# Kernel optimization log

Measured on AMD Instinct MI355X. Metric: run time of the kernel, lower is better.

Reference implementation:

```python
import jax, jax.numpy as jnp
import numpy as np

B, N, DIM = 4, 4096, 1024
HEADS, DIM_HEAD, BSZ, EPS = 8, 64, 16, 1e-8
INNER = HEADS * DIM_HEAD


def setup_inputs() -> dict:
    key = jax.random.key(0)
    k1, k2, k3 = jax.random.split(key, 3)
    x = jax.random.normal(k1, (B, N, DIM), dtype=jnp.float32)
    # torch nn.Linear weights are [out, in]; scale ~ fan_in^-0.5 for stable exp()
    w_qkv = jax.random.normal(k2, (3 * INNER, DIM), dtype=jnp.float32) * (DIM ** -0.5)
    w_out = jax.random.normal(k3, (DIM, INNER), dtype=jnp.float32) * (INNER ** -0.5)
    b_out = jnp.zeros((DIM,), dtype=jnp.float32)
    return {"x": x, "w_qkv": w_qkv, "w_out": w_out, "b_out": b_out}


def _to_bh(t, b, n):
    # 'b n (h d) -> (b h) n d'
    return t.reshape(b, n, HEADS, DIM_HEAD).transpose(0, 2, 1, 3).reshape(b * HEADS, n, DIM_HEAD)


def _to_blocks(t):
    # 'b (n z) d -> b n z d'
    return t.reshape(t.shape[0], -1, BSZ, DIM_HEAD)


def _calc_Y_and_A(qb, kb, vb):
    S = jnp.einsum('bnid,bnjd->bnij', qb, kb)   # block-local scores
    A = jnp.exp(S)
    y = jnp.einsum('bnij,bnjd->bnid', A, vb)
    return y.reshape(y.shape[0], -1, DIM_HEAD), A.sum(-1).reshape(A.shape[0], -1)


def _hattention(x, w_qkv, w_out, b_out):
    b, n, _ = x.shape
    qkv = x @ w_qkv.T
    q, k, v = jnp.split(qkv, 3, axis=-1)
    q, k, v = (_to_bh(t, b, n) for t in (q, k, v))
    q = q * (DIM_HEAD ** -0.5)

    num_levels = int(np.log2(n // BSZ)) - 1
    qkvs = [(q, k, v)]
    for _ in range(num_levels):
        q = q.reshape(q.shape[0], -1, 2, DIM_HEAD).mean(axis=2)
        k = k.reshape(k.shape[0], -1, 2, DIM_HEAD).mean(axis=2)
        v = v.reshape(v.shape[0], -1, 2, DIM_HEAD).sum(axis=2)
        qkvs.append((q, k, v))
    top_level = qkvs[0]
    coarse_levels = qkvs[1:][::-1]  # coarsest first

    Ys = []
    for (ql, kl, vl) in coarse_levels:
        qb, kb, vb = map(_to_blocks, (ql, kl, vl))
        bh, nb = kb.shape[0], kb.shape[1]
        # flip sibling key blocks: 'b (n r) z d' with r=2 reversed
        kb = kb.reshape(bh, nb // 2, 2, BSZ, DIM_HEAD)[:, :, ::-1].reshape(bh, nb, BSZ, DIM_HEAD)
        Ys.append(_calc_Y_and_A(qb, kb, vb))
    Ys.append(_calc_Y_and_A(*map(_to_blocks, top_level)))

    Y, A = Ys[0]
    for y_l, a_l in Ys[1:]:
        Y = jnp.repeat(Y, 2, axis=1) + y_l
        A = jnp.repeat(A, 2, axis=1) + a_l

    out = Y / (A + EPS)[..., None]
    # '(b h) n d -> b n (h d)'
    out = out.reshape(b, HEADS, n, DIM_HEAD).transpose(0, 2, 1, 3).reshape(b, n, INNER)
    return out @ w_out.T + b_out


def reference(x, w_qkv, w_out, b_out):
    return _hattention(x, w_qkv, w_out, b_out)
```

## Files before the change

kernel.cpp:

```cpp
#include <hip/hip_runtime.h>
#include <hip/hip_bf16.h>


typedef __bf16 bf16x8 __attribute__((ext_vector_type(8)));
typedef float floatx4 __attribute__((ext_vector_type(4)));
typedef unsigned short ushortx8 __attribute__((ext_vector_type(8)));
typedef unsigned int uintx4 __attribute__((ext_vector_type(4)));

#define ROWS_PER_BH 8160

__device__ __forceinline__ void g2lds16(const void* g, void* l) {
  __builtin_amdgcn_global_load_lds(
      (const __attribute__((address_space(1))) void*)g,
      (__attribute__((address_space(3))) void*)l, 16, 0, 0);
}

__device__ __forceinline__ unsigned short f2bu(float x) {
  __hip_bfloat16 h = __float2bfloat16(x);
  return *(unsigned short*)&h;
}
__device__ __forceinline__ float bu2f(unsigned short u) {
  __hip_bfloat16 h = *(__hip_bfloat16*)&u;
  return __bfloat162float(h);
}

__global__ __launch_bounds__(256) void f2b_kernel(const float* __restrict__ s,
                                                  __hip_bfloat16* __restrict__ d,
                                                  int n) {
  int i0 = (blockIdx.x * 256 + threadIdx.x) * 4;
  if (i0 + 3 < n) {
    float4 v = *(const float4*)(s + i0);
    d[i0 + 0] = __float2bfloat16(v.x);
    d[i0 + 1] = __float2bfloat16(v.y);
    d[i0 + 2] = __float2bfloat16(v.z);
    d[i0 + 3] = __float2bfloat16(v.w);
  }
}

template <int K>
__device__ __forceinline__ void gemm_core(const unsigned short* __restrict__ A,
                                          const unsigned short* __restrict__ B,
                                          unsigned short* ldsA, unsigned short* ldsB,
                                          int tM, int tN, floatx4 acc[4][4]) {
  const int tid = threadIdx.x;
  const int lane = tid & 63, w = tid >> 6;
  const int wm = w >> 1, wn = w & 1;
  const int lr = lane >> 3;
  const int gch = (lane & 7) ^ lr;
  const unsigned short* Ag = A + (size_t)(tM + w * 32 + lr) * K + gch * 8;
  const unsigned short* Bg = B + (size_t)(tN + w * 32 + lr) * K + gch * 8;
  unsigned short* lA = &ldsA[w * 2048 + lane * 8];
  unsigned short* lB = &ldsB[w * 2048 + lane * 8];

  const int rA = wm * 64 + (lane & 15);
  const int rB = wn * 64 + (lane & 15);
  const int quad = lane >> 4;
  const int sw = lane & 7;

  for (int kt = 0; kt < K; kt += 64) {
    __syncthreads();
#pragma unroll
    for (int c = 0; c < 4; c++) {
      g2lds16(Ag + (size_t)(c * 8) * K + kt, lA + c * 512);
      g2lds16(Bg + (size_t)(c * 8) * K + kt, lB + c * 512);
    }
    __syncthreads();
#pragma unroll
    for (int kk = 0; kk < 2; kk++) {
      bf16x8 af[4], bv[4];
#pragma unroll
      for (int i = 0; i < 4; i++)
        af[i] = *(const bf16x8*)&ldsA[(rA + i * 16) * 64 + (((kk * 4 + quad) ^ sw) * 8)];
#pragma unroll
      for (int j = 0; j < 4; j++)
        bv[j] = *(const bf16x8*)&ldsB[(rB + j * 16) * 64 + (((kk * 4 + quad) ^ sw) * 8)];
#pragma unroll
      for (int i = 0; i < 4; i++)
#pragma unroll
        for (int j = 0; j < 4; j++)
          acc[i][j] = __builtin_amdgcn_mfma_f32_16x16x32_bf16(af[i], bv[j], acc[i][j], 0, 0, 0);
    }
  }
}

__global__ __launch_bounds__(256) void gemm_qkv_kernel(
    const unsigned short* __restrict__ A,
    const unsigned short* __restrict__ B,
    __hip_bfloat16* __restrict__ qp, __hip_bfloat16* __restrict__ kp,
    __hip_bfloat16* __restrict__ vp) {
  __shared__ unsigned short ldsA[128 * 64];
  __shared__ unsigned short ldsB[128 * 64];
  const int lane = threadIdx.x & 63, w = threadIdx.x >> 6;
  const int wm = w >> 1, wn = w & 1;
  const int tM = blockIdx.x * 128, tN = blockIdx.y * 128;

  floatx4 acc[4][4];
#pragma unroll
  for (int i = 0; i < 4; i++)
#pragma unroll
    for (int j = 0; j < 4; j++) acc[i][j] = (floatx4){0.f, 0.f, 0.f, 0.f};

  gemm_core<1024>(A, B, ldsA, ldsB, tM, tN, acc);

  const int quad = lane >> 4;
#pragma unroll
  for (int i = 0; i < 4; i++) {
#pragma unroll
    for (int j = 0; j < 4; j++) {
      const int c = tN + wn * 64 + j * 16 + (lane & 15);
      const int tensor = c >> 9;
      const int rem = c & 511;
      const int h = rem >> 6, d = rem & 63;
      __hip_bfloat16* dstbuf = (tensor == 0) ? qp : ((tensor == 1) ? kp : vp);
      const float scale = (tensor == 0) ? 0.125f : 1.0f;
#pragma unroll
      for (int r = 0; r < 4; r++) {
        const int m = tM + wm * 64 + i * 16 + quad * 4 + r;
        const int b = m >> 12, n = m & 4095;
        size_t dst = ((size_t)(b * 8 + h) * ROWS_PER_BH + n) * 64 + d;
        dstbuf[dst] = __float2bfloat16(acc[i][j][r] * scale);
      }
    }
  }
}

__global__ __launch_bounds__(256) void gemm_out_kernel(
    const unsigned short* __restrict__ A,
    const unsigned short* __restrict__ B,
    const float* __restrict__ bias, float* __restrict__ out) {
  __shared__ unsigned short ldsA[128 * 64];
  __shared__ unsigned short ldsB[128 * 64];
  const int lane = threadIdx.x & 63, w = threadIdx.x >> 6;
  const int wm = w >> 1, wn = w & 1;
  const int tM = blockIdx.x * 128, tN = blockIdx.y * 128;

  floatx4 acc[4][4];
#pragma unroll
  for (int i = 0; i < 4; i++)
#pragma unroll
    for (int j = 0; j < 4; j++) acc[i][j] = (floatx4){0.f, 0.f, 0.f, 0.f};

  gemm_core<512>(A, B, ldsA, ldsB, tM, tN, acc);

  const int quad = lane >> 4;
#pragma unroll
  for (int i = 0; i < 4; i++) {
#pragma unroll
    for (int j = 0; j < 4; j++) {
      const int c = tN + wn * 64 + j * 16 + (lane & 15);
      const float bb = bias[c];
#pragma unroll
      for (int r = 0; r < 4; r++) {
        const int m = tM + wm * 64 + i * 16 + quad * 4 + r;
        out[(size_t)m * 1024 + c] = acc[i][j][r] + bb;
      }
    }
  }
}

__global__ __launch_bounds__(256) void pyramid_all_kernel(
    __hip_bfloat16* __restrict__ qp, __hip_bfloat16* __restrict__ kp,
    __hip_bfloat16* __restrict__ vp) {
  __shared__ unsigned short qs[128 * 64], ks[128 * 64], vs[128 * 64];
  const int bh = blockIdx.x >> 5;
  const int chunk = blockIdx.x & 31;
  const int tid = threadIdx.x;
  const size_t base = (size_t)bh * ROWS_PER_BH;
  const size_t g0 = (base + chunk * 128) * 64;
  const unsigned short* qg = (const unsigned short*)qp;
  const unsigned short* kg = (const unsigned short*)kp;
  const unsigned short* vg = (const unsigned short*)vp;
#pragma unroll
  for (int c = 0; c < 4; c++) {
    int off = c * 2048 + tid * 8;
    *(ushortx8*)&qs[off] = *(const ushortx8*)(qg + g0 + off);
    *(ushortx8*)&ks[off] = *(const ushortx8*)(kg + g0 + off);
    *(ushortx8*)&vs[off] = *(const ushortx8*)(vg + g0 + off);
  }
  const int offs[8] = {0, 4096, 6144, 7168, 7680, 7936, 8064, 8128};
#pragma unroll
  for (int l = 1; l <= 7; l++) {
    __syncthreads();
    const int nOut = 128 >> l;
    for (int e = tid; e < nOut * 32; e += 256) {
      const int i = e >> 5, dp = (e & 31) * 2;
      const int a = (i << l) * 64 + dp;
      const int b = a + (1 << (l - 1)) * 64;
      unsigned short q0 = f2bu(0.5f * (bu2f(qs[a]) + bu2f(qs[b])));
      unsigned short q1 = f2bu(0.5f * (bu2f(qs[a + 1]) + bu2f(qs[b + 1])));
      unsigned short k0 = f2bu(0.5f * (bu2f(ks[a]) + bu2f(ks[b])));
      unsigned short k1 = f2bu(0.5f * (bu2f(ks[a + 1]) + bu2f(ks[b + 1])));
      unsigned short v0 = f2bu(bu2f(vs[a]) + bu2f(vs[b]));
      unsigned short v1 = f2bu(bu2f(vs[a + 1]) + bu2f(vs[b + 1]));
      qs[a] = q0; qs[a + 1] = q1;
      ks[a] = k0; ks[a + 1] = k1;
      vs[a] = v0; vs[a + 1] = v1;
      const size_t grow = (base + offs[l] + (size_t)chunk * nOut + i) * 64 + dp;
      *(unsigned int*)((unsigned short*)qp + grow) = (unsigned int)q0 | ((unsigned int)q1 << 16);
      *(unsigned int*)((unsigned short*)kp + grow) = (unsigned int)k0 | ((unsigned int)k1 << 16);
      *(unsigned int*)((unsigned short*)vp + grow) = (unsigned int)v0 | ((unsigned int)v1 << 16);
    }
  }
}

__global__ __launch_bounds__(256) void attn_kernel(
    const unsigned short* __restrict__ qp, const unsigned short* __restrict__ kp,
    const unsigned short* __restrict__ vp, __hip_bfloat16* __restrict__ yall,
    float* __restrict__ aall) {
  __shared__ __align__(16) unsigned short vT[4][64 * 24];
  const int w = threadIdx.x >> 6, lane = threadIdx.x & 63;
  const int g = blockIdx.x * 4 + w;
  if (g >= 510) return;
  const int bh = blockIdx.y;
  int level, blk;
  if (g < 256)      { level = 0; blk = g; }
  else if (g < 384) { level = 1; blk = g - 256; }
  else if (g < 448) { level = 2; blk = g - 384; }
  else if (g < 480) { level = 3; blk = g - 448; }
  else if (g < 496) { level = 4; blk = g - 480; }
  else if (g < 504) { level = 5; blk = g - 496; }
  else if (g < 508) { level = 6; blk = g - 504; }
  else              { level = 7; blk = g - 508; }
  const int ro = 8192 - (8192 >> level);
  const int kblk = (level == 0) ? blk : (blk ^ 1);
  const int m = lane & 15, q = lane >> 4;
  const size_t qbase = ((size_t)bh * ROWS_PER_BH + ro + blk * 16) * 64;
  const size_t kbase = ((size_t)bh * ROWS_PER_BH + ro + kblk * 16) * 64;

  const bf16x8 ka0 = *(const bf16x8*)(kp + kbase + m * 64 + q * 8);
  const bf16x8 ka1 = *(const bf16x8*)(kp + kbase + m * 64 + 32 + q * 8);
  const bf16x8 qb0 = *(const bf16x8*)(qp + qbase + m * 64 + q * 8);
  const bf16x8 qb1 = *(const bf16x8*)(qp + qbase + m * 64 + 32 + q * 8);

  const ushortx8 v0 = *(const ushortx8*)(vp + qbase + m * 64 + q * 16);
  const ushortx8 v1 = *(const ushortx8*)(vp + qbase + m * 64 + q * 16 + 8);
  unsigned short* vtw = vT[w];
#pragma unroll
  for (int j = 0; j < 8; j++) vtw[(q * 16 + j) * 24 + m] = v0[j];
#pragma unroll
  for (int j = 0; j < 8; j++) vtw[(q * 16 + 8 + j) * 24 + m] = v1[j];

  floatx4 s = (floatx4){0.f, 0.f, 0.f, 0.f};
  s = __builtin_amdgcn_mfma_f32_16x16x32_bf16(ka0, qb0, s, 0, 0, 0);
  s = __builtin_amdgcn_mfma_f32_16x16x32_bf16(ka1, qb1, s, 0, 0, 0);

  unsigned short pb0 = f2bu(__expf(s[0])), pb1 = f2bu(__expf(s[1]));
  unsigned short pb2 = f2bu(__expf(s[2])), pb3 = f2bu(__expf(s[3]));
  float asum = bu2f(pb0) + bu2f(pb1) + bu2f(pb2) + bu2f(pb3);
  asum += __shfl_xor(asum, 16, 64);
  asum += __shfl_xor(asum, 32, 64);
  const size_t arow = (size_t)bh * ROWS_PER_BH + ro + blk * 16;
  if (q == 0) aall[arow + m] = asum;

  unsigned int d0 = (unsigned int)pb0 | ((unsigned int)pb1 << 16);
  unsigned int d1 = (unsigned int)pb2 | ((unsigned int)pb3 << 16);
  const int s0l = m + 32 * (q & 1);
  unsigned int u0 = __shfl(d0, s0l, 64);
  unsigned int u1 = __shfl(d1, s0l, 64);
  unsigned int u2 = __shfl(d0, s0l + 16, 64);
  unsigned int u3 = __shfl(d1, s0l + 16, 64);
  union { uintx4 i; bf16x8 b; } pau;
  pau.i = (q < 2) ? (uintx4){u0, u1, u2, u3} : (uintx4){0u, 0u, 0u, 0u};
  const bf16x8 pa = pau.b;

#pragma unroll
  for (int c = 0; c < 4; c++) {
    union { uintx4 i; bf16x8 b; } bvu;
    bvu.i = (uintx4){0u, 0u, 0u, 0u};
    if (q < 2) bvu.b = *(const bf16x8*)&vtw[(c * 16 + m) * 24 + q * 8];
    floatx4 y = (floatx4){0.f, 0.f, 0.f, 0.f};
    y = __builtin_amdgcn_mfma_f32_16x16x32_bf16(pa, bvu.b, y, 0, 0, 0);
#pragma unroll
    for (int r = 0; r < 4; r++)
      yall[(arow + q * 4 + r) * 64 + c * 16 + m] = __float2bfloat16(y[r]);
  }
}

__global__ __launch_bounds__(256) void combine_kernel(
    const unsigned short* __restrict__ yall, const float* __restrict__ aall,
    __hip_bfloat16* __restrict__ Ub) {
  int idx = blockIdx.x * 256 + threadIdx.x;
  int d = idx & 63;
  int i = (idx >> 6) & 4095;
  int bh = idx >> 18;
  size_t base = (size_t)bh * ROWS_PER_BH;
  float Y = 0.f, Aa = 0.f;
#pragma unroll
  for (int l = 0; l < 8; l++) {
    int r = (8192 - (8192 >> l)) + (i >> l);
    Y += bu2f(yall[(base + r) * 64 + d]);
    Aa += aall[base + r];
  }
  float u = Y / (Aa + 1e-8f);
  int b = bh >> 3, h = bh & 7;
  size_t m = (size_t)b * 4096 + i;
  Ub[m * 512 + (size_t)h * 64 + d] = __float2bfloat16(u);
}

extern "C" void kernel_launch(void* const* d_in, const int* in_sizes, int n_in,
                              void* d_out, int out_size, void* d_ws, size_t ws_size,
                              hipStream_t stream) {
  const float* x     = (const float*)d_in[0];
  const float* w_qkv = (const float*)d_in[1];
  const float* w_out = (const float*)d_in[2];
  const float* b_out = (const float*)d_in[3];
  float* out = (float*)d_out;

  char* ws = (char*)d_ws;
  __hip_bfloat16* xb    = (__hip_bfloat16*)(ws + 0);
  __hip_bfloat16* wqkvb = (__hip_bfloat16*)(ws + 33554432);
  __hip_bfloat16* wob   = (__hip_bfloat16*)(ws + 36700160);
  __hip_bfloat16* qp    = (__hip_bfloat16*)(ws + 37748736);
  __hip_bfloat16* kp    = (__hip_bfloat16*)(ws + 71172096);
  __hip_bfloat16* vp    = (__hip_bfloat16*)(ws + 104595456);
  __hip_bfloat16* yall  = (__hip_bfloat16*)(ws + 138018816);
  float* aall           = (float*)(ws + 171442176);
  __hip_bfloat16* Ub    = (__hip_bfloat16*)(ws + 172486656);

  f2b_kernel<<<16384, 256, 0, stream>>>(x, xb, 16777216);
  f2b_kernel<<<1536, 256, 0, stream>>>(w_qkv, wqkvb, 1572864);
  f2b_kernel<<<512, 256, 0, stream>>>(w_out, wob, 524288);

  gemm_qkv_kernel<<<dim3(128, 12), 256, 0, stream>>>(
      (const unsigned short*)xb, (const unsigned short*)wqkvb, qp, kp, vp);

  pyramid_all_kernel<<<1024, 256, 0, stream>>>(qp, kp, vp);

  attn_kernel<<<dim3(128, 32), 256, 0, stream>>>(
      (const unsigned short*)qp, (const unsigned short*)kp,
      (const unsigned short*)vp, yall, aall);

  combine_kernel<<<32768, 256, 0, stream>>>((const unsigned short*)yall, aall, Ub);

  gemm_out_kernel<<<dim3(128, 8), 256, 0, stream>>>(
      (const unsigned short*)Ub, (const unsigned short*)wob, b_out, out);
}
```

Before: 276.7 us.

## Use 256x256 double-buffered pipelined GEMM core for QKV and output projections

Replaces the 128x128 single-buffered GEMM core with a 256x256 tile per 512-thread block. It double-buffers LDS, prefetches the next K tiles during MFMA phases, and raises wave priority around the MFMA bursts. The goal is more operand reuse per LDS load and hiding global-to-LDS latency. The cost is 128KB of LDS per block and far fewer blocks, which can limit occupancy and leave tail imbalance in the QKV grid.

```diff
diff --git a/kernel.cpp b/kernel.cpp
--- a/kernel.cpp
+++ b/kernel.cpp
@@ -22,6 +22,15 @@
 __device__ __forceinline__ float bu2f(unsigned short u) {
   __hip_bfloat16 h = *(__hip_bfloat16*)&u;
   return __bfloat162float(h);
+}
+
+__device__ __forceinline__ void wg_barrier() {
+  asm volatile("" ::: "memory");
+  __builtin_amdgcn_s_barrier();
+  asm volatile("" ::: "memory");
+}
+__device__ __forceinline__ void lgk0() {
+  asm volatile("s_waitcnt lgkmcnt(0)" ::: "memory");
 }
 
 __global__ __launch_bounds__(256) void f2b_kernel(const float* __restrict__ s,
@@ -38,121 +47,197 @@
 }
 
 template <int K>
-__device__ __forceinline__ void gemm_core(const unsigned short* __restrict__ A,
-                                          const unsigned short* __restrict__ B,
-                                          unsigned short* ldsA, unsigned short* ldsB,
-                                          int tM, int tN, floatx4 acc[4][4]) {
+__device__ __forceinline__ void gemm256_core(const unsigned short* __restrict__ A,
+                                             const unsigned short* __restrict__ B,
+                                             unsigned short* lds, int tM, int tN,
+                                             floatx4 acc[8][4]) {
   const int tid = threadIdx.x;
-  const int lane = tid & 63, w = tid >> 6;
-  const int wm = w >> 1, wn = w & 1;
-  const int lr = lane >> 3;
-  const int gch = (lane & 7) ^ lr;
-  const unsigned short* Ag = A + (size_t)(tM + w * 32 + lr) * K + gch * 8;
-  const unsigned short* Bg = B + (size_t)(tN + w * 32 + lr) * K + gch * 8;
-  unsigned short* lA = &ldsA[w * 2048 + lane * 8];
-  unsigned short* lB = &ldsB[w * 2048 + lane * 8];
-
-  const int rA = wm * 64 + (lane & 15);
-  const int rB = wn * 64 + (lane & 15);
-  const int quad = lane >> 4;
-  const int sw = lane & 7;
-
-  for (int kt = 0; kt < K; kt += 64) {
-    __syncthreads();
-#pragma unroll
-    for (int c = 0; c < 4; c++) {
-      g2lds16(Ag + (size_t)(c * 8) * K + kt, lA + c * 512);
-      g2lds16(Bg + (size_t)(c * 8) * K + kt, lB + c * 512);
-    }
-    __syncthreads();
-#pragma unroll
-    for (int kk = 0; kk < 2; kk++) {
-      bf16x8 af[4], bv[4];
-#pragma unroll
-      for (int i = 0; i < 4; i++)
-        af[i] = *(const bf16x8*)&ldsA[(rA + i * 16) * 64 + (((kk * 4 + quad) ^ sw) * 8)];
-#pragma unroll
-      for (int j = 0; j < 4; j++)
-        bv[j] = *(const bf16x8*)&ldsB[(rB + j * 16) * 64 + (((kk * 4 + quad) ^ sw) * 8)];
-#pragma unroll
-      for (int i = 0; i < 4; i++)
-#pragma unroll
-        for (int j = 0; j < 4; j++)
-          acc[i][j] = __builtin_amdgcn_mfma_f32_16x16x32_bf16(af[i], bv[j], acc[i][j], 0, 0, 0);
-    }
-  }
-}
-
-__global__ __launch_bounds__(256) void gemm_qkv_kernel(
+  const int lane = tid & 63;
+  const int w = tid >> 6;
+  const int wm = w >> 2, wn = w & 3;
+
+  const int srow = tid >> 3;
+  const int schunk = (tid & 7) ^ (srow & 7);
+  const unsigned short* Ab = A + (size_t)(tM + srow) * K + schunk * 8;
+  const unsigned short* Bb = B + (size_t)(tN + srow) * K + schunk * 8;
+  const int ltid8 = tid * 8;
+
+  auto stage = [&](const unsigned short* gbase, unsigned short* lbase, int half, int kt) {
+    const unsigned short* g = gbase + (size_t)(half * 128) * K + kt;
+    unsigned short* l = lbase + half * 8192 + ltid8;
+    g2lds16(g, l);
+    g2lds16(g + (size_t)64 * K, l + 4096);
+  };
+
+  stage(Ab, lds, 0, 0); stage(Ab, lds, 1, 0);
+  stage(Bb, lds + 16384, 0, 0); stage(Bb, lds + 16384, 1, 0);
+  stage(Ab, lds + 32768, 0, 64); stage(Ab, lds + 32768, 1, 64);
+  stage(Bb, lds + 49152, 0, 64); stage(Bb, lds + 49152, 1, 64);
+  asm volatile("s_waitcnt vmcnt(8)" ::: "memory");
+  wg_barrier();
+
+  const int frow = lane & 15, quad = lane >> 4, sw = frow & 7;
+  const int arbase = (wm * 128 + frow) * 64;
+  const int brbase = (wn * 64 + frow) * 64;
+  const int NT = K / 64;
+
+  for (int t = 0; t < NT; ++t) {
+    unsigned short* lA = lds + ((t & 1) << 15);
+    unsigned short* lB = lA + 16384;
+    const int ktn = (t + 2) * 64;
+    const bool st = (t + 2) < NT;
+
+    bf16x8 bfr[4][2], a01[2][2][2];
+#pragma unroll
+    for (int nf = 0; nf < 4; nf++)
+#pragma unroll
+      for (int kk = 0; kk < 2; kk++)
+        bfr[nf][kk] = *(const bf16x8*)&lB[brbase + nf * 1024 + (((kk * 4 + quad) ^ sw) * 8)];
+#pragma unroll
+    for (int q = 0; q < 2; q++)
+#pragma unroll
+      for (int mf2 = 0; mf2 < 2; mf2++)
+#pragma unroll
+        for (int kk = 0; kk < 2; kk++)
+          a01[q][mf2][kk] = *(const bf16x8*)&lA[arbase + (q * 2 + mf2) * 1024 +
+                                                (((kk * 4 + quad) ^ sw) * 8)];
+    wg_barrier();
+    lgk0();
+    __builtin_amdgcn_s_setprio(1);
+#pragma unroll
+    for (int mf2 = 0; mf2 < 2; mf2++)
+#pragma unroll
+      for (int nf = 0; nf < 4; nf++)
+#pragma unroll
+        for (int kk = 0; kk < 2; kk++)
+          acc[mf2][nf] = __builtin_amdgcn_mfma_f32_16x16x32_bf16(
+              a01[0][mf2][kk], bfr[nf][kk], acc[mf2][nf], 0, 0, 0);
+    __builtin_amdgcn_s_setprio(0);
+    wg_barrier();
+
+    bf16x8 a23[2][2][2];
+#pragma unroll
+    for (int q = 0; q < 2; q++)
+#pragma unroll
+      for (int mf2 = 0; mf2 < 2; mf2++)
+#pragma unroll
+        for (int kk = 0; kk < 2; kk++)
+          a23[q][mf2][kk] = *(const bf16x8*)&lA[arbase + (4 + q * 2 + mf2) * 1024 +
+                                                (((kk * 4 + quad) ^ sw) * 8)];
+    if (st) { stage(Bb, lB, 0, ktn); stage(Bb, lB, 1, ktn); }
+    wg_barrier();
+    lgk0();
+    __builtin_amdgcn_s_setprio(1);
+#pragma unroll
+    for (int mf2 = 0; mf2 < 2; mf2++)
+#pragma unroll
+      for (int nf = 0; nf < 4; nf++)
+#pragma unroll
+        for (int kk = 0; kk < 2; kk++)
+          acc[2 + mf2][nf] = __builtin_amdgcn_mfma_f32_16x16x32_bf16(
+              a01[1][mf2][kk], bfr[nf][kk], acc[2 + mf2][nf], 0, 0, 0);
+    __builtin_amdgcn_s_setprio(0);
+    wg_barrier();
+
+    if (st) stage(Ab, lA, 0, ktn);
+    wg_barrier();
+    __builtin_amdgcn_s_setprio(1);
+#pragma unroll
+    for (int mf2 = 0; mf2 < 2; mf2++)
+#pragma unroll
+      for (int nf = 0; nf < 4; nf++)
+#pragma unroll
+        for (int kk = 0; kk < 2; kk++)
+          acc[4 + mf2][nf] = __builtin_amdgcn_mfma_f32_16x16x32_bf16(
+              a23[0][mf2][kk], bfr[nf][kk], acc[4 + mf2][nf], 0, 0, 0);
+    __builtin_amdgcn_s_setprio(0);
+    wg_barrier();
+
+    if (st) stage(Ab, lA, 1, ktn);
+    wg_barrier();
+    __builtin_amdgcn_s_setprio(1);
+#pragma unroll
+    for (int mf2 = 0; mf2 < 2; mf2++)
+#pragma unroll
+      for (int nf = 0; nf < 4; nf++)
+#pragma unroll
+        for (int kk = 0; kk < 2; kk++)
+          acc[6 + mf2][nf] = __builtin_amdgcn_mfma_f32_16x16x32_bf16(
+              a23[1][mf2][kk], bfr[nf][kk], acc[6 + mf2][nf], 0, 0, 0);
+    __builtin_amdgcn_s_setprio(0);
+    if (st) asm volatile("s_waitcnt vmcnt(6)" ::: "memory");
+    else    asm volatile("s_waitcnt vmcnt(0)" ::: "memory");
+    wg_barrier();
+  }
+}
+
+__global__ __launch_bounds__(512, 2) void gemm_qkv_kernel(
     const unsigned short* __restrict__ A,
     const unsigned short* __restrict__ B,
     __hip_bfloat16* __restrict__ qp, __hip_bfloat16* __restrict__ kp,
     __hip_bfloat16* __restrict__ vp) {
-  __shared__ unsigned short ldsA[128 * 64];
-  __shared__ unsigned short ldsB[128 * 64];
+  __shared__ __align__(16) unsigned short lds[65536];
   const int lane = threadIdx.x & 63, w = threadIdx.x >> 6;
-  const int wm = w >> 1, wn = w & 1;
-  const int tM = blockIdx.x * 128, tN = blockIdx.y * 128;
-
-  floatx4 acc[4][4];
-#pragma unroll
-  for (int i = 0; i < 4; i++)
+  const int wm = w >> 2, wn = w & 3;
+  const int tM = blockIdx.x * 256, tN = blockIdx.y * 256;
+
+  floatx4 acc[8][4];
+#pragma unroll
+  for (int i = 0; i < 8; i++)
 #pragma unroll
     for (int j = 0; j < 4; j++) acc[i][j] = (floatx4){0.f, 0.f, 0.f, 0.f};
 
-  gemm_core<1024>(A, B, ldsA, ldsB, tM, tN, acc);
-
-  const int quad = lane >> 4;
-#pragma unroll
-  for (int i = 0; i < 4; i++) {
-#pragma unroll
-    for (int j = 0; j < 4; j++) {
-      const int c = tN + wn * 64 + j * 16 + (lane & 15);
-      const int tensor = c >> 9;
-      const int rem = c & 511;
-      const int h = rem >> 6, d = rem & 63;
-      __hip_bfloat16* dstbuf = (tensor == 0) ? qp : ((tensor == 1) ? kp : vp);
-      const float scale = (tensor == 0) ? 0.125f : 1.0f;
+  gemm256_core<1024>(A, B, lds, tM, tN, acc);
+
+  const int quad = lane >> 4, m15 = lane & 15;
+  const int cbase = tN + wn * 64;
+  const int tensor = cbase >> 9;
+  const int h = (cbase & 511) >> 6;
+  __hip_bfloat16* dstbuf = (tensor == 0) ? qp : ((tensor == 1) ? kp : vp);
+  const float scale = (tensor == 0) ? 0.125f : 1.0f;
+#pragma unroll
+  for (int mf = 0; mf < 8; mf++) {
+#pragma unroll
+    for (int nf = 0; nf < 4; nf++) {
 #pragma unroll
       for (int r = 0; r < 4; r++) {
-        const int m = tM + wm * 64 + i * 16 + quad * 4 + r;
+        const int m = tM + wm * 128 + mf * 16 + quad * 4 + r;
         const int b = m >> 12, n = m & 4095;
-        size_t dst = ((size_t)(b * 8 + h) * ROWS_PER_BH + n) * 64 + d;
-        dstbuf[dst] = __float2bfloat16(acc[i][j][r] * scale);
+        dstbuf[((size_t)(b * 8 + h) * ROWS_PER_BH + n) * 64 + nf * 16 + m15] =
+            __float2bfloat16(acc[mf][nf][r] * scale);
       }
     }
   }
 }
 
-__global__ __launch_bounds__(256) void gemm_out_kernel(
+__global__ __launch_bounds__(512, 2) void gemm_out_kernel(
     const unsigned short* __restrict__ A,
     const unsigned short* __restrict__ B,
     const float* __restrict__ bias, float* __restrict__ out) {
-  __shared__ unsigned short ldsA[128 * 64];
-  __shared__ unsigned short ldsB[128 * 64];
+  __shared__ __align__(16) unsigned short lds[65536];
   const int lane = threadIdx.x & 63, w = threadIdx.x >> 6;
-  const int wm = w >> 1, wn = w & 1;
-  const int tM = blockIdx.x * 128, tN = blockIdx.y * 128;
-
-  floatx4 acc[4][4];
-#pragma unroll
-  for (int i = 0; i < 4; i++)
+  const int wm = w >> 2, wn = w & 3;
+  const int tM = blockIdx.x * 256, tN = blockIdx.y * 256;
+
+  floatx4 acc[8][4];
+#pragma unroll
+  for (int i = 0; i < 8; i++)
 #pragma unroll
     for (int j = 0; j < 4; j++) acc[i][j] = (floatx4){0.f, 0.f, 0.f, 0.f};
 
-  gemm_core<512>(A, B, ldsA, ldsB, tM, tN, acc);
-
-  const int quad = lane >> 4;
-#pragma unroll
-  for (int i = 0; i < 4; i++) {
-#pragma unroll
-    for (int j = 0; j < 4; j++) {
-      const int c = tN + wn * 64 + j * 16 + (lane & 15);
+  gemm256_core<512>(A, B, lds, tM, tN, acc);
+
+  const int quad = lane >> 4, m15 = lane & 15;
+#pragma unroll
+  for (int mf = 0; mf < 8; mf++) {
+#pragma unroll
+    for (int nf = 0; nf < 4; nf++) {
+      const int c = tN + wn * 64 + nf * 16 + m15;
       const float bb = bias[c];
 #pragma unroll
       for (int r = 0; r < 4; r++) {
-        const int m = tM + wm * 64 + i * 16 + quad * 4 + r;
-        out[(size_t)m * 1024 + c] = acc[i][j][r] + bb;
+        const int m = tM + wm * 128 + mf * 16 + quad * 4 + r;
+        out[(size_t)m * 1024 + c] = acc[mf][nf][r] + bb;
       }
     }
   }
@@ -321,7 +406,7 @@
   f2b_kernel<<<1536, 256, 0, stream>>>(w_qkv, wqkvb, 1572864);
   f2b_kernel<<<512, 256, 0, stream>>>(w_out, wob, 524288);
 
-  gemm_qkv_kernel<<<dim3(128, 12), 256, 0, stream>>>(
+  gemm_qkv_kernel<<<dim3(64, 6), 512, 0, stream>>>(
       (const unsigned short*)xb, (const unsigned short*)wqkvb, qp, kp, vp);
 
   pyramid_all_kernel<<<1024, 256, 0, stream>>>(qp, kp, vp);
@@ -332,6 +417,6 @@
 
   combine_kernel<<<32768, 256, 0, stream>>>((const unsigned short*)yall, aall, Ub);
 
-  gemm_out_kernel<<<dim3(128, 8), 256, 0, stream>>>(
+  gemm_out_kernel<<<dim3(64, 4), 512, 0, stream>>>(
       (const unsigned short*)Ub, (const unsigned short*)wob, b_out, out);
 }
```

New measurement: 285.6 us. 3.2% more time.
